# Performance work log

Measured on AMD Instinct MI355X. Metric: run time of the kernel, lower is better.

## Reference

```python
import jax, jax.numpy as jnp
import numpy as np

N, C, D = 32768, 2048, 512

def setup_inputs() -> dict:
    key = jax.random.key(0)
    k1, k2, k3 = jax.random.split(key, 3)
    X = jax.random.normal(k1, (N, D), dtype=jnp.float32)
    muK = jax.random.normal(k2, (C, D), dtype=jnp.float32)
    # counts per class; zeros mark 'unvisited' classes exercising the masking path
    cK = jax.random.randint(k3, (C,), 0, 3).astype(jnp.float32)
    return {"X": X, "muK": muK, "cK": cK}

def reference(X, muK, cK):
    # find_dists(A=muK, B=X): dist[i, j] = sum_d (muK[j, d] - X[i, d])**2, scores = -dist
    # avoids materializing the N x C x D broadcast intermediate of the original).
    x2 = jnp.sum(X * X, axis=1, keepdims=True)          # (N, 1)
    m2 = jnp.sum(muK * muK, axis=1)                     # (C,)
    scores = -(x2 + m2[None, :] - 2.0 * (X @ muK.T))    # (N, C)
    # unvisited classes (cK == 0) get per-row min score minus 1
    min_col = jnp.min(scores, axis=1, keepdims=True) - 1.0  # (N, 1)
    scores = jnp.where((cK == 0.0)[None, :], min_col, scores)
    # predict(..., return_probas=True) as used in evaluate_
    return jax.nn.softmax(scores, axis=1)
```

## Files before the change

### kernel.cpp

```cpp
#include <hip/hip_runtime.h>
#include <cfloat>

#define N_ROWS 32768
#define N_CLS  2048
#define DIM    512

typedef __attribute__((ext_vector_type(8))) short short8;
typedef __attribute__((ext_vector_type(4))) short short4v;
typedef __attribute__((ext_vector_type(4))) float f32x4;

__device__ __forceinline__ unsigned f2bf_bits(float x) {
    union { float f; unsigned u; } a; a.f = x;
    return (a.u + 0x7fffu + ((a.u >> 16) & 1u)) >> 16;
}
__device__ __forceinline__ float bf_to_f(unsigned bits) {
    union { unsigned u; float f; } a; a.u = bits << 16;
    return a.f;
}
__device__ __forceinline__ void split_bf(float x, short &h, short &l) {
    unsigned hb = f2bf_bits(x);
    h = (short)hb;
    float r = x - bf_to_f(hb);
    l = (short)f2bf_bits(r);
}

__global__ __launch_bounds__(256) void split_kernel(const float* __restrict__ src,
                                                    short* __restrict__ hi,
                                                    short* __restrict__ lo) {
    int idx = blockIdx.x * 256 + threadIdx.x;
    float4 v = ((const float4*)src)[idx];
    short h0, h1, h2, h3, l0, l1, l2, l3;
    split_bf(v.x, h0, l0); split_bf(v.y, h1, l1);
    split_bf(v.z, h2, l2); split_bf(v.w, h3, l3);
    ((short4v*)hi)[idx] = (short4v){h0, h1, h2, h3};
    ((short4v*)lo)[idx] = (short4v){l0, l1, l2, l3};
}

__global__ __launch_bounds__(256) void m2_kernel(const float* __restrict__ muK,
                                                 float* __restrict__ m2) {
    const int j = blockIdx.x;
    const int t = threadIdx.x;
    const float* r = muK + (size_t)j * DIM;
    float a = r[t], b = r[t + 256];
    float s = a * a + b * b;
    for (int off = 32; off; off >>= 1) s += __shfl_xor(s, off);
    __shared__ float sw[4];
    if ((t & 63) == 0) sw[t >> 6] = s;
    __syncthreads();
    if (t == 0) m2[j] = sw[0] + sw[1] + sw[2] + sw[3];
}

#define GLDS16(g, l) __builtin_amdgcn_global_load_lds( \
    (const __attribute__((address_space(1))) unsigned int*)(g), \
    (__attribute__((address_space(3))) unsigned int*)(l), 16, 0, 0)

__global__ __launch_bounds__(256) void gemm_kernel(const short* __restrict__ Xh,
                                                   const short* __restrict__ Xl,
                                                   const short* __restrict__ Mh,
                                                   const short* __restrict__ Ml,
                                                   const float* __restrict__ m2,
                                                   float* __restrict__ S) {
    __shared__ __align__(16) short As[128 * 32];
    __shared__ __align__(16) short Bs[128 * 32];

    const int tid  = threadIdx.x;
    const int n0   = blockIdx.x * 128;
    const int m0   = blockIdx.y * 128;
    const int w    = tid >> 6;
    const int lane = tid & 63;
    const int wm   = (w >> 1) * 64;
    const int wn   = (w & 1) * 64;
    const int l16  = lane & 15;
    const int quad = lane >> 4;

    const int c0 = w * 128 + lane;
    const int c1 = c0 + 64;
    const size_t ga0 = (size_t)(m0 + (c0 >> 2)) * DIM + (c0 & 3) * 8;
    const size_t ga1 = (size_t)(m0 + (c1 >> 2)) * DIM + (c1 & 3) * 8;
    const size_t gb0 = (size_t)(n0 + (c0 >> 2)) * DIM + (c0 & 3) * 8;
    const size_t gb1 = (size_t)(n0 + (c1 >> 2)) * DIM + (c1 & 3) * 8;

    f32x4 acc[4][4];
#pragma unroll
    for (int mt = 0; mt < 4; ++mt)
#pragma unroll
        for (int nt = 0; nt < 4; ++nt)
            acc[mt][nt] = (f32x4){0.f, 0.f, 0.f, 0.f};

#pragma unroll 1
    for (int seg = 0; seg < 3; ++seg) {
        const short* Ap = (seg == 2) ? Xl : Xh;
        const short* Bp = (seg == 1) ? Ml : Mh;
#pragma unroll 1
        for (int kt2 = 0; kt2 < 16; ++kt2) {
            const int kk = kt2 * 32;
            __syncthreads();
            GLDS16(Ap + ga0 + kk, &As[c0 * 8]);
            GLDS16(Ap + ga1 + kk, &As[c1 * 8]);
            GLDS16(Bp + gb0 + kk, &Bs[c0 * 8]);
            GLDS16(Bp + gb1 + kk, &Bs[c1 * 8]);
            __syncthreads();

            short8 ah[4];
#pragma unroll
            for (int mt = 0; mt < 4; ++mt)
                ah[mt] = *(const short8*)&As[(wm + mt * 16 + l16) * 32 + quad * 8];
#pragma unroll
            for (int nt = 0; nt < 4; ++nt) {
                short8 bf = *(const short8*)&Bs[(wn + nt * 16 + l16) * 32 + quad * 8];
#pragma unroll
                for (int mt = 0; mt < 4; ++mt)
                    acc[mt][nt] = __builtin_amdgcn_mfma_f32_16x16x32_bf16(ah[mt], bf, acc[mt][nt], 0, 0, 0);
            }
        }
    }

#pragma unroll
    for (int nt = 0; nt < 4; ++nt) {
        int col = n0 + wn + nt * 16 + l16;
        float mm = m2[col];
#pragma unroll
        for (int mt = 0; mt < 4; ++mt) {
            int rbase = m0 + wm + mt * 16 + quad * 4;
#pragma unroll
            for (int r = 0; r < 4; ++r)
                S[(size_t)(rbase + r) * N_CLS + col] = 2.0f * acc[mt][nt][r] - mm;
        }
    }
}

#define LDR 40
__global__ __launch_bounds__(256) void gemm_fallback(const float* __restrict__ X,
                                                     const float* __restrict__ muK,
                                                     const float* __restrict__ m2,
                                                     float* __restrict__ S) {
    __shared__ __align__(16) short Ah[128 * LDR];
    __shared__ __align__(16) short Al[128 * LDR];
    __shared__ __align__(16) short Bh[128 * LDR];
    __shared__ __align__(16) short Bl[128 * LDR];
    const int tid  = threadIdx.x;
    const int n0   = blockIdx.x * 128;
    const int m0   = blockIdx.y * 128;
    const int w    = tid >> 6;
    const int lane = tid & 63;
    const int wm   = (w >> 1) * 64;
    const int wn   = (w & 1) * 64;
    const int l16  = lane & 15;
    const int quad = lane >> 4;
    f32x4 acc[4][4];
#pragma unroll
    for (int mt = 0; mt < 4; ++mt)
#pragma unroll
        for (int nt = 0; nt < 4; ++nt)
            acc[mt][nt] = (f32x4){0.f, 0.f, 0.f, 0.f};
    for (int kt = 0; kt < DIM; kt += 32) {
        __syncthreads();
#pragma unroll
        for (int i = 0; i < 4; ++i) {
            int idx = tid + 256 * i;
            int row = idx >> 3;
            int c4  = (idx & 7) * 4;
            float4 fa = *(const float4*)(X + (size_t)(m0 + row) * DIM + kt + c4);
            float4 fb = *(const float4*)(muK + (size_t)(n0 + row) * DIM + kt + c4);
            short h0, h1, h2, h3, l0, l1, l2, l3;
            split_bf(fa.x, h0, l0); split_bf(fa.y, h1, l1);
            split_bf(fa.z, h2, l2); split_bf(fa.w, h3, l3);
            *(short4v*)&Ah[row * LDR + c4] = (short4v){h0, h1, h2, h3};
            *(short4v*)&Al[row * LDR + c4] = (short4v){l0, l1, l2, l3};
            split_bf(fb.x, h0, l0); split_bf(fb.y, h1, l1);
            split_bf(fb.z, h2, l2); split_bf(fb.w, h3, l3);
            *(short4v*)&Bh[row * LDR + c4] = (short4v){h0, h1, h2, h3};
            *(short4v*)&Bl[row * LDR + c4] = (short4v){l0, l1, l2, l3};
        }
        __syncthreads();
        short8 ah[4], al[4];
#pragma unroll
        for (int mt = 0; mt < 4; ++mt) {
            int r = wm + mt * 16 + l16;
            ah[mt] = *(const short8*)&Ah[r * LDR + quad * 8];
            al[mt] = *(const short8*)&Al[r * LDR + quad * 8];
        }
#pragma unroll
        for (int nt = 0; nt < 4; ++nt) {
            int r = wn + nt * 16 + l16;
            short8 bh = *(const short8*)&Bh[r * LDR + quad * 8];
            short8 bl = *(const short8*)&Bl[r * LDR + quad * 8];
#pragma unroll
            for (int mt = 0; mt < 4; ++mt)
                acc[mt][nt] = __builtin_amdgcn_mfma_f32_16x16x32_bf16(ah[mt], bh, acc[mt][nt], 0, 0, 0);
#pragma unroll
            for (int mt = 0; mt < 4; ++mt)
                acc[mt][nt] = __builtin_amdgcn_mfma_f32_16x16x32_bf16(ah[mt], bl, acc[mt][nt], 0, 0, 0);
#pragma unroll
            for (int mt = 0; mt < 4; ++mt)
                acc[mt][nt] = __builtin_amdgcn_mfma_f32_16x16x32_bf16(al[mt], bh, acc[mt][nt], 0, 0, 0);
        }
    }
#pragma unroll
    for (int nt = 0; nt < 4; ++nt) {
        int col = n0 + wn + nt * 16 + l16;
        float mm = m2[col];
#pragma unroll
        for (int mt = 0; mt < 4; ++mt) {
            int rbase = m0 + wm + mt * 16 + quad * 4;
#pragma unroll
            for (int r = 0; r < 4; ++r)
                S[(size_t)(rbase + r) * N_CLS + col] = 2.0f * acc[mt][nt][r] - mm;
        }
    }
}

__global__ __launch_bounds__(256) void softmax_kernel(float* __restrict__ S,
                                                      const float* __restrict__ cK) {
    const int row  = blockIdx.x * 4 + (threadIdx.x >> 6);
    const int lane = threadIdx.x & 63;
    f32x4* p = (f32x4*)(S + (size_t)row * N_CLS);
    const float4* ck4 = (const float4*)cK;

    f32x4 v[8];
    unsigned msk = 0;
    float mn = FLT_MAX, mx = -FLT_MAX;
#pragma unroll
    for (int i = 0; i < 8; ++i) {
        int c = i * 64 + lane;
        f32x4 s = __builtin_nontemporal_load(&p[c]);
        float4 k = ck4[c];
        v[i] = s;
        if (k.x == 0.f) msk |= 1u << (i * 4 + 0); else mx = fmaxf(mx, s.x);
        if (k.y == 0.f) msk |= 1u << (i * 4 + 1); else mx = fmaxf(mx, s.y);
        if (k.z == 0.f) msk |= 1u << (i * 4 + 2); else mx = fmaxf(mx, s.z);
        if (k.w == 0.f) msk |= 1u << (i * 4 + 3); else mx = fmaxf(mx, s.w);
        mn = fminf(mn, fminf(fminf(s.x, s.y), fminf(s.z, s.w)));
    }
    for (int off = 32; off; off >>= 1) {
        mn = fminf(mn, __shfl_xor(mn, off));
        mx = fmaxf(mx, __shfl_xor(mx, off));
    }
    if (mx == -FLT_MAX) mx = mn - 1.0f;
    const float fill = mn - 1.0f;

    float sum = 0.f;
#pragma unroll
    for (int i = 0; i < 8; ++i) {
        f32x4 s = v[i];
        s.x = __expf(((msk >> (i * 4 + 0)) & 1u ? fill : s.x) - mx);
        s.y = __expf(((msk >> (i * 4 + 1)) & 1u ? fill : s.y) - mx);
        s.z = __expf(((msk >> (i * 4 + 2)) & 1u ? fill : s.z) - mx);
        s.w = __expf(((msk >> (i * 4 + 3)) & 1u ? fill : s.w) - mx);
        sum += s.x + s.y + s.z + s.w;
        v[i] = s;
    }
    for (int off = 32; off; off >>= 1) sum += __shfl_xor(sum, off);
    const float inv = 1.0f / sum;
#pragma unroll
    for (int i = 0; i < 8; ++i) {
        f32x4 s = v[i] * inv;
        __builtin_nontemporal_store(s, &p[i * 64 + lane]);
    }
}

extern "C" void kernel_launch(void* const* d_in, const int* in_sizes, int n_in,
                              void* d_out, int out_size, void* d_ws, size_t ws_size,
                              hipStream_t stream) {
    const float* X   = (const float*)d_in[0];
    const float* muK = (const float*)d_in[1];
    const float* cK  = (const float*)d_in[2];
    float* out = (float*)d_out;

    const size_t XN = (size_t)N_ROWS * DIM;
    const size_t MN = (size_t)N_CLS * DIM;
    short* Xh = (short*)d_ws;
    short* Xl = Xh + XN;
    short* Mh = Xl + XN;
    short* Ml = Mh + MN;
    float* m2 = (float*)(Ml + MN);
    const size_t need = (2 * XN + 2 * MN) * sizeof(short) + N_CLS * sizeof(float);

    if (ws_size >= need) {
        split_kernel<<<(int)(XN / 4 / 256), 256, 0, stream>>>(X, Xh, Xl);
        split_kernel<<<(int)(MN / 4 / 256), 256, 0, stream>>>(muK, Mh, Ml);
        m2_kernel<<<N_CLS, 256, 0, stream>>>(muK, m2);
        dim3 grid(N_CLS / 128, N_ROWS / 128);
        gemm_kernel<<<grid, 256, 0, stream>>>(Xh, Xl, Mh, Ml, m2, out);
    } else {
        float* m2f = (float*)d_ws;
        m2_kernel<<<N_CLS, 256, 0, stream>>>(muK, m2f);
        dim3 grid(N_CLS / 128, N_ROWS / 128);
        gemm_fallback<<<grid, 256, 0, stream>>>(X, muK, m2f, out);
    }
    softmax_kernel<<<N_ROWS / 4, 256, 0, stream>>>(out, cK);
}
```

Baseline: 620.7 us.

## Swizzle GEMM LDS tiles and process four rows per wave in softmax

```diff
diff --git a/kernel.cpp b/kernel.cpp
--- a/kernel.cpp
+++ b/kernel.cpp
@@ -75,10 +75,12 @@
 
     const int c0 = w * 128 + lane;
     const int c1 = c0 + 64;
-    const size_t ga0 = (size_t)(m0 + (c0 >> 2)) * DIM + (c0 & 3) * 8;
-    const size_t ga1 = (size_t)(m0 + (c1 >> 2)) * DIM + (c1 & 3) * 8;
-    const size_t gb0 = (size_t)(n0 + (c0 >> 2)) * DIM + (c0 & 3) * 8;
-    const size_t gb1 = (size_t)(n0 + (c1 >> 2)) * DIM + (c1 & 3) * 8;
+    const size_t ga0 = (size_t)(m0 + (c0 >> 2)) * DIM + (size_t)(((c0 & 3) ^ ((c0 >> 3) & 3)) * 8);
+    const size_t ga1 = (size_t)(m0 + (c1 >> 2)) * DIM + (size_t)(((c1 & 3) ^ ((c1 >> 3) & 3)) * 8);
+    const size_t gb0 = (size_t)(n0 + (c0 >> 2)) * DIM + (size_t)(((c0 & 3) ^ ((c0 >> 3) & 3)) * 8);
+    const size_t gb1 = (size_t)(n0 + (c1 >> 2)) * DIM + (size_t)(((c1 & 3) ^ ((c1 >> 3) & 3)) * 8);
+
+    const int sw = (quad ^ ((l16 >> 1) & 3)) * 8;
 
     f32x4 acc[4][4];
 #pragma unroll
@@ -104,10 +106,10 @@
             short8 ah[4];
 #pragma unroll
             for (int mt = 0; mt < 4; ++mt)
-                ah[mt] = *(const short8*)&As[(wm + mt * 16 + l16) * 32 + quad * 8];
+                ah[mt] = *(const short8*)&As[(wm + mt * 16 + l16) * 32 + sw];
 #pragma unroll
             for (int nt = 0; nt < 4; ++nt) {
-                short8 bf = *(const short8*)&Bs[(wn + nt * 16 + l16) * 32 + quad * 8];
+                short8 bf = *(const short8*)&Bs[(wn + nt * 16 + l16) * 32 + sw];
 #pragma unroll
                 for (int mt = 0; mt < 4; ++mt)
                     acc[mt][nt] = __builtin_amdgcn_mfma_f32_16x16x32_bf16(ah[mt], bf, acc[mt][nt], 0, 0, 0);
@@ -210,27 +212,23 @@
     }
 }
 
-__global__ __launch_bounds__(256) void softmax_kernel(float* __restrict__ S,
-                                                      const float* __restrict__ cK) {
-    const int row  = blockIdx.x * 4 + (threadIdx.x >> 6);
-    const int lane = threadIdx.x & 63;
-    f32x4* p = (f32x4*)(S + (size_t)row * N_CLS);
-    const float4* ck4 = (const float4*)cK;
-
-    f32x4 v[8];
-    unsigned msk = 0;
+__device__ __forceinline__ void sm_load_row(float* S, int row, int lane, f32x4* v) {
+    const f32x4* pi = (const f32x4*)(S + (size_t)row * N_CLS);
+#pragma unroll
+    for (int i = 0; i < 8; ++i) v[i] = pi[i * 64 + lane];
+}
+
+__device__ __forceinline__ void sm_compute_store(float* S, int row, int lane,
+                                                 unsigned msk, f32x4* v) {
     float mn = FLT_MAX, mx = -FLT_MAX;
 #pragma unroll
     for (int i = 0; i < 8; ++i) {
-        int c = i * 64 + lane;
-        f32x4 s = __builtin_nontemporal_load(&p[c]);
-        float4 k = ck4[c];
-        v[i] = s;
-        if (k.x == 0.f) msk |= 1u << (i * 4 + 0); else mx = fmaxf(mx, s.x);
-        if (k.y == 0.f) msk |= 1u << (i * 4 + 1); else mx = fmaxf(mx, s.y);
-        if (k.z == 0.f) msk |= 1u << (i * 4 + 2); else mx = fmaxf(mx, s.z);
-        if (k.w == 0.f) msk |= 1u << (i * 4 + 3); else mx = fmaxf(mx, s.w);
+        f32x4 s = v[i];
         mn = fminf(mn, fminf(fminf(s.x, s.y), fminf(s.z, s.w)));
+        if (!((msk >> (i * 4 + 0)) & 1u)) mx = fmaxf(mx, s.x);
+        if (!((msk >> (i * 4 + 1)) & 1u)) mx = fmaxf(mx, s.y);
+        if (!((msk >> (i * 4 + 2)) & 1u)) mx = fmaxf(mx, s.z);
+        if (!((msk >> (i * 4 + 3)) & 1u)) mx = fmaxf(mx, s.w);
     }
     for (int off = 32; off; off >>= 1) {
         mn = fminf(mn, __shfl_xor(mn, off));
@@ -252,11 +250,41 @@
     }
     for (int off = 32; off; off >>= 1) sum += __shfl_xor(sum, off);
     const float inv = 1.0f / sum;
+    f32x4* po = (f32x4*)(S + (size_t)row * N_CLS);
 #pragma unroll
     for (int i = 0; i < 8; ++i) {
         f32x4 s = v[i] * inv;
-        __builtin_nontemporal_store(s, &p[i * 64 + lane]);
-    }
+        __builtin_nontemporal_store(s, &po[i * 64 + lane]);
+    }
+}
+
+__global__ __launch_bounds__(256) void softmax_kernel(float* __restrict__ S,
+                                                      const float* __restrict__ cK) {
+    const int w    = threadIdx.x >> 6;
+    const int lane = threadIdx.x & 63;
+    const float4* ck4 = (const float4*)cK;
+
+    unsigned msk = 0;
+#pragma unroll
+    for (int i = 0; i < 8; ++i) {
+        float4 k = ck4[i * 64 + lane];
+        if (k.x == 0.f) msk |= 1u << (i * 4 + 0);
+        if (k.y == 0.f) msk |= 1u << (i * 4 + 1);
+        if (k.z == 0.f) msk |= 1u << (i * 4 + 2);
+        if (k.w == 0.f) msk |= 1u << (i * 4 + 3);
+    }
+
+    const int r0 = blockIdx.x * 16 + w * 4;
+    f32x4 va[8], vb[8];
+
+    sm_load_row(S, r0 + 0, lane, va);
+    sm_load_row(S, r0 + 1, lane, vb);
+    sm_compute_store(S, r0 + 0, lane, msk, va);
+    sm_load_row(S, r0 + 2, lane, va);
+    sm_compute_store(S, r0 + 1, lane, msk, vb);
+    sm_load_row(S, r0 + 3, lane, vb);
+    sm_compute_store(S, r0 + 2, lane, msk, va);
+    sm_compute_store(S, r0 + 3, lane, msk, vb);
 }
 
 extern "C" void kernel_launch(void* const* d_in, const int* in_sizes, int n_in,
@@ -269,24 +297,24 @@
 
     const size_t XN = (size_t)N_ROWS * DIM;
     const size_t MN = (size_t)N_CLS * DIM;
-    short* Xh = (short*)d_ws;
-    short* Xl = Xh + XN;
-    short* Mh = Xl + XN;
-    short* Ml = Mh + MN;
-    float* m2 = (float*)(Ml + MN);
     const size_t need = (2 * XN + 2 * MN) * sizeof(short) + N_CLS * sizeof(float);
 
+    dim3 grid(N_CLS / 128, N_ROWS / 128);
+
     if (ws_size >= need) {
+        short* Xh = (short*)d_ws;
+        short* Xl = Xh + XN;
+        short* Mh = Xl + XN;
+        short* Ml = Mh + MN;
+        float* m2 = (float*)(Ml + MN);
         split_kernel<<<(int)(XN / 4 / 256), 256, 0, stream>>>(X, Xh, Xl);
         split_kernel<<<(int)(MN / 4 / 256), 256, 0, stream>>>(muK, Mh, Ml);
         m2_kernel<<<N_CLS, 256, 0, stream>>>(muK, m2);
-        dim3 grid(N_CLS / 128, N_ROWS / 128);
         gemm_kernel<<<grid, 256, 0, stream>>>(Xh, Xl, Mh, Ml, m2, out);
     } else {
         float* m2f = (float*)d_ws;
         m2_kernel<<<N_CLS, 256, 0, stream>>>(muK, m2f);
-        dim3 grid(N_CLS / 128, N_ROWS / 128);
         gemm_fallback<<<grid, 256, 0, stream>>>(X, muK, m2f, out);
     }
-    softmax_kernel<<<N_ROWS / 4, 256, 0, stream>>>(out, cK);
-}
+    softmax_kernel<<<N_ROWS / 16, 256, 0, stream>>>(out, cK);
+}
```

Result: no change. 626.5 us (+0.9%).
